# Kernel optimization log

Measured on AMD Instinct MI355X. Metric: run time of the kernel, lower is better.

The kernel has to match this reference:

```python
import jax, jax.numpy as jnp
import numpy as np

DIM = 2048
N_HEADS = 32
N_KV_HEADS = 8
HEAD_DIM = DIM // N_HEADS  # 64
ROPE_BASE = 10000
B, S = 2, 2048


def rope_cos_sin(seq_len, head_dim, base=ROPE_BASE):
    # theta: [head_dim//2]
    theta = 1.0 / (base ** (jnp.arange(0, head_dim, 2, dtype=jnp.float32) / head_dim))
    idx_theta = jnp.arange(seq_len, dtype=jnp.float32)[:, None] * theta[None, :]  # [s, hd/2]
    return jnp.cos(idx_theta), jnp.sin(idx_theta)


def apply_rope(t, cos, sin):
    # t: [b, s, h, hd]; cos/sin: [s, hd/2]
    b, s, h, hd = t.shape
    t2 = t.reshape(b, s, h, hd // 2, 2)
    x0, x1 = t2[..., 0], t2[..., 1]
    c = cos[None, :, None, :]
    sn = sin[None, :, None, :]
    out = jnp.stack([x0 * c - x1 * sn, x1 * c + x0 * sn], axis=-1)
    return out.reshape(b, s, h, hd)


def setup_inputs() -> dict:
    key = jax.random.key(0)
    k1, k2, k3 = jax.random.split(key, 3)
    x = jax.random.normal(k1, (B, S, DIM), dtype=jnp.float32)
    # packed projection weight, stored [in, out]; torch Linear would be its transpose
    packed = DIM + 2 * N_KV_HEADS * HEAD_DIM  # 3072
    w_qkv = jax.random.normal(k2, (DIM, packed), dtype=jnp.float32) * (DIM ** -0.5)
    w_out = jax.random.normal(k3, (DIM, DIM), dtype=jnp.float32) * (DIM ** -0.5)
    return {"x": x, "w_qkv": w_qkv, "w_out": w_out}


def reference(x, w_qkv, w_out):
    b, s, e = x.shape
    hd = HEAD_DIM
    kv_size = N_KV_HEADS * hd
    qkv = x @ w_qkv  # [b, s, dim + 2*kv]
    q = qkv[..., :DIM].reshape(b, s, N_HEADS, hd)
    k = qkv[..., DIM:DIM + kv_size].reshape(b, s, N_KV_HEADS, hd)
    v = qkv[..., DIM + kv_size:].reshape(b, s, N_KV_HEADS, hd)

    cos, sin = rope_cos_sin(s, hd)
    q = apply_rope(q, cos, sin)
    k = apply_rope(k, cos, sin)

    # GQA: group query heads per kv head
    g = N_HEADS // N_KV_HEADS
    q = q.transpose(0, 2, 1, 3).reshape(b, N_KV_HEADS, g, s, hd)  # [b, kh, g, s, hd]
    k = k.transpose(0, 2, 1, 3)  # [b, kh, s, hd]
    v = v.transpose(0, 2, 1, 3)

    scale = 1.0 / jnp.sqrt(jnp.float32(hd))
    scores = jnp.einsum('bkgqd,bktd->bkgqt', q, k) * scale  # [b, kh, g, s, s]
    causal = jnp.tril(jnp.ones((s, s), dtype=bool))
    scores = jnp.where(causal[None, None, None], scores, jnp.finfo(scores.dtype).min)
    probs = jax.nn.softmax(scores, axis=-1)
    attn = jnp.einsum('bkgqt,bktd->bkgqd', probs, v)  # [b, kh, g, s, hd]
    attn = attn.reshape(b, N_HEADS, s, hd).transpose(0, 2, 1, 3).reshape(b, s, DIM)
    return attn @ w_out
```

## Files before the change

### kernel.cpp

```cpp
#include <hip/hip_runtime.h>
#include <hip/hip_bf16.h>
#include <cstdint>
#include <cstddef>

#define DIME 2048
#define NH 32
#define NKV 8
#define HD 64
#define BB 2
#define SSEQ 2048
#define PACKED (DIME + 2*NKV*HD)
#define MTOT (BB*SSEQ)

typedef __attribute__((ext_vector_type(8))) short bf16x8;
typedef __attribute__((ext_vector_type(4))) float f32x4;
typedef __attribute__((ext_vector_type(16))) float f32x16;
typedef __attribute__((ext_vector_type(4))) unsigned u32x4;

__device__ __forceinline__ short f2b(float f) {
  unsigned u = __builtin_bit_cast(unsigned, f);
  u += 0x7fffu + ((u >> 16) & 1u);
  return (short)(u >> 16);
}
__device__ __forceinline__ float b2f(short s) {
  unsigned u = ((unsigned)(unsigned short)s) << 16;
  return __builtin_bit_cast(float, u);
}
__device__ __forceinline__ unsigned cvt_pk(float lo, float hi) {
  unsigned r;
  asm("v_cvt_pk_bf16_f32 %0, %1, %2" : "=v"(r) : "v"(lo), "v"(hi));
  return r;
}

__device__ __forceinline__ void gload_lds16(const void* g, void* l) {
  __builtin_amdgcn_global_load_lds(
      (const __attribute__((address_space(1))) void*)g,
      (__attribute__((address_space(3))) void*)l, 16, 0, 0);
}

__global__ __launch_bounds__(256) void cast_bf16(const float* __restrict__ in,
                                                 short* __restrict__ out, int n4) {
  int i = blockIdx.x * blockDim.x + threadIdx.x;
  int stride = gridDim.x * blockDim.x;
  for (; i < n4; i += stride) {
    float4 v = ((const float4*)in)[i];
    short4 o;
    o.x = f2b(v.x); o.y = f2b(v.y); o.z = f2b(v.z); o.w = f2b(v.w);
    ((short4*)out)[i] = o;
  }
}

__global__ __launch_bounds__(256) void transpose_cast(const float* __restrict__ in,
                                                      short* __restrict__ out,
                                                      int R, int C) {
  __shared__ float tile[32][33];
  int bx = blockIdx.x * 32;
  int by = blockIdx.y * 32;
  int tx = threadIdx.x;
  int ty = threadIdx.y;
  #pragma unroll
  for (int j = 0; j < 4; ++j)
    tile[ty + j*8][tx] = in[(size_t)(by + ty + j*8) * C + bx + tx];
  __syncthreads();
  #pragma unroll
  for (int j = 0; j < 4; ++j)
    out[(size_t)(bx + ty + j*8) * R + by + tx] = f2b(tile[tx][ty + j*8]);
}

__global__ __launch_bounds__(256) void rope_table(float* __restrict__ ctab,
                                                  float* __restrict__ stab) {
  int t = blockIdx.x * blockDim.x + threadIdx.x;
  int s = t >> 5, i = t & 31;
  float theta = 1.0f / powf(10000.0f, (float)(2 * i) * (1.0f / (float)HD));
  float ang = (float)s * theta;
  float sn, cs;
  sincosf(ang, &sn, &cs);
  ctab[t] = cs;
  stab[t] = sn;
}

template<bool BF16_OUT>
__global__ __launch_bounds__(256) void gemm_bt(const short* __restrict__ A,
                                               const short* __restrict__ BT,
                                               void* __restrict__ Cout,
                                               int M, int N, int K) {
  __shared__ __align__(16) short lds[2][2][2][4096];
  const int tid = threadIdx.x;
  const int l = tid & 63, w = tid >> 6;
  const int lr = l & 15, lg = l >> 4;
  const int wm = w >> 1, wn = w & 1;
  const int bm = blockIdx.x * 128, bn = blockIdx.y * 128;
  const int NT = K >> 6;

  const int srow = w * 16 + (l >> 2);
  const int scol = (l & 3) * 8;

  auto stage = [&](int t, int c) {
    const int k0 = t << 6;
    #pragma unroll
    for (int s = 0; s < 2; ++s)
      #pragma unroll
      for (int j = 0; j < 2; ++j) {
        gload_lds16(A  + (size_t)(bm + j * 64 + srow) * K + k0 + s * 32 + scol,
                    &lds[c][0][s][(j * 256 + w * 64) * 8]);
        gload_lds16(BT + (size_t)(bn + j * 64 + srow) * K + k0 + s * 32 + scol,
                    &lds[c][1][s][(j * 256 + w * 64) * 8]);
      }
  };

  f32x4 acc[4][4];
  #pragma unroll
  for (int m = 0; m < 4; ++m)
    #pragma unroll
    for (int n = 0; n < 4; ++n) {
      f32x4 z = {0.f, 0.f, 0.f, 0.f};
      acc[m][n] = z;
    }

  stage(0, 0);
  stage(1, 1);
  asm volatile("s_waitcnt vmcnt(8)" ::: "memory");
  __builtin_amdgcn_sched_barrier(0);
  __builtin_amdgcn_s_barrier();

  for (int t = 0; t < NT; ++t) {
    const int c = t & 1;
    bf16x8 af[4][2], bfr[4][2];
    #pragma unroll
    for (int m = 0; m < 4; ++m)
      #pragma unroll
      for (int ks = 0; ks < 2; ++ks)
        af[m][ks] = *(const bf16x8*)&lds[c][0][ks][((wm * 64 + m * 16 + lr) * 4 + lg) * 8];
    #pragma unroll
    for (int n = 0; n < 4; ++n)
      #pragma unroll
      for (int ks = 0; ks < 2; ++ks)
        bfr[n][ks] = *(const bf16x8*)&lds[c][1][ks][((wn * 64 + n * 16 + lr) * 4 + lg) * 8];
    asm volatile("s_waitcnt lgkmcnt(0)" ::: "memory");
    __builtin_amdgcn_sched_barrier(0);
    __builtin_amdgcn_s_barrier();
    if (t + 2 < NT) stage(t + 2, c);
    __builtin_amdgcn_s_setprio(1);
    #pragma unroll
    for (int m = 0; m < 4; ++m)
      #pragma unroll
      for (int n = 0; n < 4; ++n) {
        acc[m][n] = __builtin_amdgcn_mfma_f32_16x16x32_bf16(af[m][0], bfr[n][0], acc[m][n], 0, 0, 0);
        acc[m][n] = __builtin_amdgcn_mfma_f32_16x16x32_bf16(af[m][1], bfr[n][1], acc[m][n], 0, 0, 0);
      }
    __builtin_amdgcn_s_setprio(0);
    if (t + 2 < NT) {
      asm volatile("s_waitcnt vmcnt(8)" ::: "memory");
    } else if (t + 1 < NT) {
      asm volatile("s_waitcnt vmcnt(0)" ::: "memory");
    }
    __builtin_amdgcn_sched_barrier(0);
    __builtin_amdgcn_s_barrier();
  }

  #pragma unroll
  for (int m = 0; m < 4; ++m)
    #pragma unroll
    for (int n = 0; n < 4; ++n)
      #pragma unroll
      for (int r = 0; r < 4; ++r) {
        int row = bm + wm * 64 + m * 16 + lg * 4 + r;
        int col = bn + wn * 64 + n * 16 + lr;
        if (BF16_OUT)
          ((short*)Cout)[(size_t)row * N + col] = f2b(acc[m][n][r]);
        else
          ((float*)Cout)[(size_t)row * N + col] = acc[m][n][r];
      }
}

__global__ __launch_bounds__(256) void rope_split(const short* __restrict__ qkv,
                                                  const float* __restrict__ ctab,
                                                  const float* __restrict__ stab,
                                                  short* __restrict__ Qo,
                                                  short* __restrict__ Ko) {
  int w = threadIdx.x >> 6, l = threadIdx.x & 63;
  int job = blockIdx.x * 4 + w;
  int b = job / (SSEQ * 40);
  int rem = job % (SSEQ * 40);
  int s = rem / 40;
  int hh = rem % 40;
  size_t base = (size_t)(b * SSEQ + s) * PACKED;
  int off = (hh < 32) ? (hh * HD + l) : (DIME + (hh - 32) * HD + l);
  float x = b2f(qkv[base + off]);
  float other = __shfl_xor(x, 1);
  int i = l >> 1;
  float cs = ctab[s * 32 + i], sn = stab[s * 32 + i];
  float o = (l & 1) ? (x * cs + other * sn) : (x * cs - other * sn);
  if (hh < 32) {
    o *= 0.180336880f;
    Qo[((size_t)(b * NH + hh) * SSEQ + s) * HD + l] = f2b(o);
  } else {
    Ko[((size_t)(b * NKV + (hh - 32)) * SSEQ + s) * HD + l] = f2b(o);
  }
}

__global__ __launch_bounds__(256) void v_transpose(const short* __restrict__ qkv,
                                                   short* __restrict__ VT) {
  __shared__ __align__(16) short tile[64][72];
  int bkv = blockIdx.x >> 5;
  int st = blockIdx.x & 31;
  int s0 = st * 64;
  int t = threadIdx.x;
  int srow = t >> 2, dq = (t & 3) * 16;
  size_t rowbase = (size_t)((bkv >> 3) * SSEQ + s0 + srow) * PACKED
                   + (DIME + NKV * HD) + (bkv & 7) * HD + dq;
  bf16x8 v0 = *(const bf16x8*)&qkv[rowbase];
  bf16x8 v1 = *(const bf16x8*)&qkv[rowbase + 8];
  #pragma unroll
  for (int j = 0; j < 8; ++j) tile[dq + j][srow] = v0[j];
  #pragma unroll
  for (int j = 0; j < 8; ++j) tile[dq + 8 + j][srow] = v1[j];
  __syncthreads();
  int d = t >> 2, sq = (t & 3) * 16;
  size_t obase = ((size_t)bkv * HD + d) * SSEQ + s0 + sq;
  *(bf16x8*)&VT[obase]     = *(const bf16x8*)&tile[d][sq];
  *(bf16x8*)&VT[obase + 8] = *(const bf16x8*)&tile[d][sq + 8];
}

__global__ __launch_bounds__(512) void attn_fwd(const short* __restrict__ Q,
                                                const short* __restrict__ K,
                                                const short* __restrict__ VT,
                                                short* __restrict__ Aout) {
  __shared__ __align__(16) short Ks[2][4096];
  __shared__ __align__(16) short Vs[2][4096];
  const int tid = threadIdx.x, l = tid & 63, w = tid >> 6;
  const int l31 = l & 31;
  const int hi = l >> 5;
  const int qb = 7 - (int)(blockIdx.x >> 6);
  const int bh = blockIdx.x & 63;
  const int b = bh >> 5, hh = bh & 31, kvh = hh >> 2;
  const short* Qp = Q + (size_t)(b * NH + hh) * SSEQ * HD;
  const short* Kp = K + (size_t)(b * NKV + kvh) * SSEQ * HD;
  const short* Vp = VT + (size_t)(b * NKV + kvh) * HD * SSEQ;
  const int q0 = qb * 256 + w * 32;
  const int qrow = q0 + l31;

  const int srow = tid >> 3;
  const int ssl = (tid & 7) ^ (srow & 7);
  auto stage = [&](int t, int c) {
    const int kv0s = t * 64;
    gload_lds16(Kp + (size_t)(kv0s + srow) * HD + ssl * 8, &Ks[c][w * 512]);
    gload_lds16(Vp + (size_t)srow * SSEQ + kv0s + ssl * 8, &Vs[c][w * 512]);
  };

  bf16x8 qf[4];
  #pragma unroll
  for (int ks = 0; ks < 4; ++ks)
    qf[ks] = *(const bf16x8*)&Qp[(size_t)qrow * HD + ks * 16 + hi * 8];

  f32x16 O0, O1;
  #pragma unroll
  for (int r = 0; r < 16; ++r) { O0[r] = 0.f; O1[r] = 0.f; }
  float lsum = 0.f;

  auto compute = [&](int c, int kv0) {
    bf16x8 kf0[4], kf1[4];
    #pragma unroll
    for (int ks = 0; ks < 4; ++ks) {
      kf0[ks] = *(const bf16x8*)&Ks[c][(l31 * 8 + (((ks << 1) + hi) ^ (l31 & 7))) * 8];
      kf1[ks] = *(const bf16x8*)&Ks[c][((32 + l31) * 8 + (((ks << 1) + hi) ^ (l31 & 7))) * 8];
    }
    f32x16 sacc[2];
    #pragma unroll
    for (int r = 0; r < 16; ++r) { sacc[0][r] = -20.f; sacc[1][r] = -20.f; }
    #pragma unroll
    for (int ks = 0; ks < 4; ++ks) {
      sacc[0] = __builtin_amdgcn_mfma_f32_32x32x16_bf16(kf0[ks], qf[ks], sacc[0], 0, 0, 0);
      sacc[1] = __builtin_amdgcn_mfma_f32_32x32x16_bf16(kf1[ks], qf[ks], sacc[1], 0, 0, 0);
    }
    bf16x8 vf0[4], vf1[4];
    #pragma unroll
    for (int ks = 0; ks < 4; ++ks) {
      vf0[ks] = *(const bf16x8*)&Vs[c][(l31 * 8 + (((ks << 1) + hi) ^ (l31 & 7))) * 8];
      vf1[ks] = *(const bf16x8*)&Vs[c][((32 + l31) * 8 + (((ks << 1) + hi) ^ (l31 & 7))) * 8];
    }
    if (kv0 + 63 > q0) {
      #pragma unroll
      for (int n = 0; n < 2; ++n)
        #pragma unroll
        for (int r = 0; r < 16; ++r) {
          int kvg = kv0 + n * 32 + ((r & 3) + 8 * (r >> 2)) + 4 * hi;
          if (kvg > qrow) sacc[n][r] = -3.0e38f;
        }
    }
    float ls0 = 0.f, ls1 = 0.f;
    #pragma unroll
    for (int r = 0; r < 16; ++r) {
      float e0 = exp2f(sacc[0][r]);
      float e1 = exp2f(sacc[1][r]);
      sacc[0][r] = e0;
      sacc[1][r] = e1;
      ls0 += e0;
      ls1 += e1;
    }
    lsum += ls0 + ls1;
    bf16x8 pa[4];
    #pragma unroll
    for (int n = 0; n < 2; ++n)
      #pragma unroll
      for (int s = 0; s < 2; ++s) {
        const int r0 = s * 8;
        unsigned A1 = cvt_pk(sacc[n][r0 + 0], sacc[n][r0 + 1]);
        unsigned B1 = cvt_pk(sacc[n][r0 + 4], sacc[n][r0 + 5]);
        unsigned A2 = cvt_pk(sacc[n][r0 + 2], sacc[n][r0 + 3]);
        unsigned B2 = cvt_pk(sacc[n][r0 + 6], sacc[n][r0 + 7]);
        unsigned shB1 = (unsigned)__shfl_xor((int)B1, 32);
        unsigned shA1 = (unsigned)__shfl_xor((int)A1, 32);
        unsigned shB2 = (unsigned)__shfl_xor((int)B2, 32);
        unsigned shA2 = (unsigned)__shfl_xor((int)A2, 32);
        u32x4 words;
        words[0] = hi ? shB1 : A1;
        words[1] = hi ? shB2 : A2;
        words[2] = hi ? B1 : shA1;
        words[3] = hi ? B2 : shA2;
        pa[n * 2 + s] = __builtin_bit_cast(bf16x8, words);
      }
    #pragma unroll
    for (int ks = 0; ks < 4; ++ks) {
      O0 = __builtin_amdgcn_mfma_f32_32x32x16_bf16(pa[ks], vf0[ks], O0, 0, 0, 0);
      O1 = __builtin_amdgcn_mfma_f32_32x32x16_bf16(pa[ks], vf1[ks], O1, 0, 0, 0);
    }
  };

  const int NT = (qb + 1) * 4;
  stage(0, 0);
  for (int t = 0; t < NT; ++t) {
    const int c = t & 1;
    if (t + 1 < NT) {
      stage(t + 1, c ^ 1);
      asm volatile("s_waitcnt vmcnt(2)" ::: "memory");
    } else {
      asm volatile("s_waitcnt vmcnt(0)" ::: "memory");
    }
    __builtin_amdgcn_sched_barrier(0);
    __builtin_amdgcn_s_barrier();
    const int kv0 = t * 64;
    if (kv0 <= q0 + 31) compute(c, kv0);
    __builtin_amdgcn_s_barrier();
  }

  lsum += __shfl_xor(lsum, 32);
  float inv = 1.0f / lsum;
  #pragma unroll
  for (int r = 0; r < 16; ++r) {
    int crow = (r & 3) + 8 * (r >> 2) + 4 * hi;
    float iq = __shfl(inv, crow);
    int qg = q0 + crow;
    size_t base = (size_t)(b * SSEQ + qg) * DIME + hh * HD;
    Aout[base + l31]      = f2b(O0[r] * iq);
    Aout[base + 32 + l31] = f2b(O1[r] * iq);
  }
}

extern "C" void kernel_launch(void* const* d_in, const int* in_sizes, int n_in,
                              void* d_out, int out_size, void* d_ws, size_t ws_size,
                              hipStream_t stream) {
  const float* x     = (const float*)d_in[0];
  const float* w_qkv = (const float*)d_in[1];
  const float* w_out = (const float*)d_in[2];
  float* out = (float*)d_out;

  char* ws = (char*)d_ws;
  size_t off = 0;
  auto alloc = [&](size_t bytes) -> void* {
    void* p = ws + off;
    off += (bytes + 255) & ~(size_t)255;
    return p;
  };
  short* xb    = (short*)alloc((size_t)MTOT * DIME * 2);
  short* wqkvT = (short*)alloc((size_t)PACKED * DIME * 2);
  short* woutT = (short*)alloc((size_t)DIME * DIME * 2);
  short* qkv   = (short*)alloc((size_t)MTOT * PACKED * 2);
  short* Qb    = (short*)alloc((size_t)BB * NH * SSEQ * HD * 2);
  short* Kb    = (short*)alloc((size_t)BB * NKV * SSEQ * HD * 2);
  short* VTb   = (short*)alloc((size_t)BB * NKV * HD * SSEQ * 2);
  float* ctab  = (float*)alloc((size_t)SSEQ * 32 * 4);
  float* stab  = (float*)alloc((size_t)SSEQ * 32 * 4);
  short* attnb = qkv;

  cast_bf16<<<2048, 256, 0, stream>>>(x, xb, MTOT * DIME / 4);
  transpose_cast<<<dim3(PACKED / 32, DIME / 32), dim3(32, 8), 0, stream>>>(w_qkv, wqkvT, DIME, PACKED);
  transpose_cast<<<dim3(DIME / 32, DIME / 32), dim3(32, 8), 0, stream>>>(w_out, woutT, DIME, DIME);
  rope_table<<<(SSEQ * 32) / 256, 256, 0, stream>>>(ctab, stab);

  gemm_bt<true><<<dim3(MTOT / 128, PACKED / 128), 256, 0, stream>>>(xb, wqkvT, qkv, MTOT, PACKED, DIME);

  rope_split<<<(BB * SSEQ * 40) / 4, 256, 0, stream>>>(qkv, ctab, stab, Qb, Kb);
  v_transpose<<<BB * NKV * (SSEQ / 64), 256, 0, stream>>>(qkv, VTb);

  attn_fwd<<<512, 512, 0, stream>>>(Qb, Kb, VTb, attnb);

  gemm_bt<false><<<dim3(MTOT / 128, DIME / 128), 256, 0, stream>>>(attnb, woutT, out, MTOT, DIME, DIME);
}
```

Before: 222.2 us.

## Fuse RoPE, head split and V transpose into QKV GEMM epilogue

The QKV projection GEMM now applies RoPE and the query scale in its epilogue and writes Q, K and transposed V directly in head-major layouts. This removes the separate rope_split and v_transpose kernels and the round trip of the packed qkv buffer through global memory. The attention grid also reorders query blocks, interleaving heavy and light causal tiles to balance the load. In exchange, the epilogue does scattered stores, shuffles and table loads, and needs a separate attention output buffer.

```diff
diff --git a/kernel.cpp b/kernel.cpp
--- a/kernel.cpp
+++ b/kernel.cpp
@@ -79,11 +79,10 @@
   stab[t] = sn;
 }
 
-template<bool BF16_OUT>
-__global__ __launch_bounds__(256) void gemm_bt(const short* __restrict__ A,
-                                               const short* __restrict__ BT,
-                                               void* __restrict__ Cout,
-                                               int M, int N, int K) {
+__global__ __launch_bounds__(256) void gemm_bt_f32(const short* __restrict__ A,
+                                                   const short* __restrict__ BT,
+                                                   float* __restrict__ Cout,
+                                                   int M, int N, int K) {
   __shared__ __align__(16) short lds[2][2][2][4096];
   const int tid = threadIdx.x;
   const int l = tid & 63, w = tid >> 6;
@@ -166,60 +165,151 @@
       for (int r = 0; r < 4; ++r) {
         int row = bm + wm * 64 + m * 16 + lg * 4 + r;
         int col = bn + wn * 64 + n * 16 + lr;
-        if (BF16_OUT)
-          ((short*)Cout)[(size_t)row * N + col] = f2b(acc[m][n][r]);
-        else
-          ((float*)Cout)[(size_t)row * N + col] = acc[m][n][r];
-      }
-}
-
-__global__ __launch_bounds__(256) void rope_split(const short* __restrict__ qkv,
-                                                  const float* __restrict__ ctab,
-                                                  const float* __restrict__ stab,
-                                                  short* __restrict__ Qo,
-                                                  short* __restrict__ Ko) {
-  int w = threadIdx.x >> 6, l = threadIdx.x & 63;
-  int job = blockIdx.x * 4 + w;
-  int b = job / (SSEQ * 40);
-  int rem = job % (SSEQ * 40);
-  int s = rem / 40;
-  int hh = rem % 40;
-  size_t base = (size_t)(b * SSEQ + s) * PACKED;
-  int off = (hh < 32) ? (hh * HD + l) : (DIME + (hh - 32) * HD + l);
-  float x = b2f(qkv[base + off]);
-  float other = __shfl_xor(x, 1);
-  int i = l >> 1;
-  float cs = ctab[s * 32 + i], sn = stab[s * 32 + i];
-  float o = (l & 1) ? (x * cs + other * sn) : (x * cs - other * sn);
-  if (hh < 32) {
-    o *= 0.180336880f;
-    Qo[((size_t)(b * NH + hh) * SSEQ + s) * HD + l] = f2b(o);
+        Cout[(size_t)row * N + col] = acc[m][n][r];
+      }
+}
+
+__global__ __launch_bounds__(256) void gemm_qkv_fused(const short* __restrict__ A,
+                                                      const short* __restrict__ BT,
+                                                      const float* __restrict__ ctab,
+                                                      const float* __restrict__ stab,
+                                                      short* __restrict__ Qo,
+                                                      short* __restrict__ Ko,
+                                                      short* __restrict__ VT) {
+  __shared__ __align__(16) short lds[2][2][2][4096];
+  const int tid = threadIdx.x;
+  const int l = tid & 63, w = tid >> 6;
+  const int lr = l & 15, lg = l >> 4;
+  const int wm = w >> 1, wn = w & 1;
+  const int bm = blockIdx.x * 128, bn = blockIdx.y * 128;
+  const int K = DIME;
+  const int NT = K >> 6;
+
+  const int srow = w * 16 + (l >> 2);
+  const int scol = (l & 3) * 8;
+
+  auto stage = [&](int t, int c) {
+    const int k0 = t << 6;
+    #pragma unroll
+    for (int s = 0; s < 2; ++s)
+      #pragma unroll
+      for (int j = 0; j < 2; ++j) {
+        gload_lds16(A  + (size_t)(bm + j * 64 + srow) * K + k0 + s * 32 + scol,
+                    &lds[c][0][s][(j * 256 + w * 64) * 8]);
+        gload_lds16(BT + (size_t)(bn + j * 64 + srow) * K + k0 + s * 32 + scol,
+                    &lds[c][1][s][(j * 256 + w * 64) * 8]);
+      }
+  };
+
+  f32x4 acc[4][4];
+  #pragma unroll
+  for (int m = 0; m < 4; ++m)
+    #pragma unroll
+    for (int n = 0; n < 4; ++n) {
+      f32x4 z = {0.f, 0.f, 0.f, 0.f};
+      acc[m][n] = z;
+    }
+
+  stage(0, 0);
+  stage(1, 1);
+  asm volatile("s_waitcnt vmcnt(8)" ::: "memory");
+  __builtin_amdgcn_sched_barrier(0);
+  __builtin_amdgcn_s_barrier();
+
+  for (int t = 0; t < NT; ++t) {
+    const int c = t & 1;
+    bf16x8 af[4][2], bfr[4][2];
+    #pragma unroll
+    for (int m = 0; m < 4; ++m)
+      #pragma unroll
+      for (int ks = 0; ks < 2; ++ks)
+        af[m][ks] = *(const bf16x8*)&lds[c][0][ks][((wm * 64 + m * 16 + lr) * 4 + lg) * 8];
+    #pragma unroll
+    for (int n = 0; n < 4; ++n)
+      #pragma unroll
+      for (int ks = 0; ks < 2; ++ks)
+        bfr[n][ks] = *(const bf16x8*)&lds[c][1][ks][((wn * 64 + n * 16 + lr) * 4 + lg) * 8];
+    asm volatile("s_waitcnt lgkmcnt(0)" ::: "memory");
+    __builtin_amdgcn_sched_barrier(0);
+    __builtin_amdgcn_s_barrier();
+    if (t + 2 < NT) stage(t + 2, c);
+    __builtin_amdgcn_s_setprio(1);
+    #pragma unroll
+    for (int m = 0; m < 4; ++m)
+      #pragma unroll
+      for (int n = 0; n < 4; ++n) {
+        acc[m][n] = __builtin_amdgcn_mfma_f32_16x16x32_bf16(af[m][0], bfr[n][0], acc[m][n], 0, 0, 0);
+        acc[m][n] = __builtin_amdgcn_mfma_f32_16x16x32_bf16(af[m][1], bfr[n][1], acc[m][n], 0, 0, 0);
+      }
+    __builtin_amdgcn_s_setprio(0);
+    if (t + 2 < NT) {
+      asm volatile("s_waitcnt vmcnt(8)" ::: "memory");
+    } else if (t + 1 < NT) {
+      asm volatile("s_waitcnt vmcnt(0)" ::: "memory");
+    }
+    __builtin_amdgcn_sched_barrier(0);
+    __builtin_amdgcn_s_barrier();
+  }
+
+  const int col0 = bn + wn * 64;
+  const int rowb = bm + wm * 64;
+  if (bn < DIME) {
+    #pragma unroll
+    for (int m = 0; m < 4; ++m)
+      #pragma unroll
+      for (int n = 0; n < 4; ++n) {
+        const int col = col0 + n * 16 + lr;
+        const int h = col >> 6, d = col & 63;
+        const int ti = d >> 1;
+        #pragma unroll
+        for (int r = 0; r < 4; ++r) {
+          const int row = rowb + m * 16 + lg * 4 + r;
+          const int bb = row >> 11, s = row & 2047;
+          float val = acc[m][n][r];
+          float oth = __shfl_xor(val, 1);
+          float cs = ctab[s * 32 + ti], snv = stab[s * 32 + ti];
+          float o = (d & 1) ? (val * cs + oth * snv) : (val * cs - oth * snv);
+          o *= 0.180336880f;
+          Qo[((size_t)(bb * NH + h) * SSEQ + s) * HD + d] = f2b(o);
+        }
+      }
+  } else if (bn < DIME + 512) {
+    #pragma unroll
+    for (int m = 0; m < 4; ++m)
+      #pragma unroll
+      for (int n = 0; n < 4; ++n) {
+        const int col = col0 + n * 16 + lr;
+        const int kvh = (col - DIME) >> 6, d = col & 63;
+        const int ti = d >> 1;
+        #pragma unroll
+        for (int r = 0; r < 4; ++r) {
+          const int row = rowb + m * 16 + lg * 4 + r;
+          const int bb = row >> 11, s = row & 2047;
+          float val = acc[m][n][r];
+          float oth = __shfl_xor(val, 1);
+          float cs = ctab[s * 32 + ti], snv = stab[s * 32 + ti];
+          float o = (d & 1) ? (val * cs + oth * snv) : (val * cs - oth * snv);
+          Ko[((size_t)(bb * NKV + kvh) * SSEQ + s) * HD + d] = f2b(o);
+        }
+      }
   } else {
-    Ko[((size_t)(b * NKV + (hh - 32)) * SSEQ + s) * HD + l] = f2b(o);
-  }
-}
-
-__global__ __launch_bounds__(256) void v_transpose(const short* __restrict__ qkv,
-                                                   short* __restrict__ VT) {
-  __shared__ __align__(16) short tile[64][72];
-  int bkv = blockIdx.x >> 5;
-  int st = blockIdx.x & 31;
-  int s0 = st * 64;
-  int t = threadIdx.x;
-  int srow = t >> 2, dq = (t & 3) * 16;
-  size_t rowbase = (size_t)((bkv >> 3) * SSEQ + s0 + srow) * PACKED
-                   + (DIME + NKV * HD) + (bkv & 7) * HD + dq;
-  bf16x8 v0 = *(const bf16x8*)&qkv[rowbase];
-  bf16x8 v1 = *(const bf16x8*)&qkv[rowbase + 8];
-  #pragma unroll
-  for (int j = 0; j < 8; ++j) tile[dq + j][srow] = v0[j];
-  #pragma unroll
-  for (int j = 0; j < 8; ++j) tile[dq + 8 + j][srow] = v1[j];
-  __syncthreads();
-  int d = t >> 2, sq = (t & 3) * 16;
-  size_t obase = ((size_t)bkv * HD + d) * SSEQ + s0 + sq;
-  *(bf16x8*)&VT[obase]     = *(const bf16x8*)&tile[d][sq];
-  *(bf16x8*)&VT[obase + 8] = *(const bf16x8*)&tile[d][sq + 8];
+    #pragma unroll
+    for (int m = 0; m < 4; ++m) {
+      const int row0 = rowb + m * 16 + lg * 4;
+      const int bb = row0 >> 11, s = row0 & 2047;
+      #pragma unroll
+      for (int n = 0; n < 4; ++n) {
+        const int cc = col0 - (DIME + 512) + n * 16 + lr;
+        const int kvh = cc >> 6, d = cc & 63;
+        short4 o4;
+        o4.x = f2b(acc[m][n][0]);
+        o4.y = f2b(acc[m][n][1]);
+        o4.z = f2b(acc[m][n][2]);
+        o4.w = f2b(acc[m][n][3]);
+        *(short4*)&VT[((size_t)(bb * NKV + kvh) * HD + d) * SSEQ + s] = o4;
+      }
+    }
+  }
 }
 
 __global__ __launch_bounds__(512) void attn_fwd(const short* __restrict__ Q,
@@ -231,7 +321,8 @@
   const int tid = threadIdx.x, l = tid & 63, w = tid >> 6;
   const int l31 = l & 31;
   const int hi = l >> 5;
-  const int qb = 7 - (int)(blockIdx.x >> 6);
+  const int j = (int)(blockIdx.x >> 6);
+  const int qb = (j < 4) ? (7 - j) : (j - 4);
   const int bh = blockIdx.x & 63;
   const int b = bh >> 5, hh = bh & 31, kvh = hh >> 2;
   const short* Qp = Q + (size_t)(b * NH + hh) * SSEQ * HD;
@@ -375,25 +466,22 @@
   short* xb    = (short*)alloc((size_t)MTOT * DIME * 2);
   short* wqkvT = (short*)alloc((size_t)PACKED * DIME * 2);
   short* woutT = (short*)alloc((size_t)DIME * DIME * 2);
-  short* qkv   = (short*)alloc((size_t)MTOT * PACKED * 2);
   short* Qb    = (short*)alloc((size_t)BB * NH * SSEQ * HD * 2);
   short* Kb    = (short*)alloc((size_t)BB * NKV * SSEQ * HD * 2);
   short* VTb   = (short*)alloc((size_t)BB * NKV * HD * SSEQ * 2);
+  short* attnb = (short*)alloc((size_t)MTOT * DIME * 2);
   float* ctab  = (float*)alloc((size_t)SSEQ * 32 * 4);
   float* stab  = (float*)alloc((size_t)SSEQ * 32 * 4);
-  short* attnb = qkv;
 
   cast_bf16<<<2048, 256, 0, stream>>>(x, xb, MTOT * DIME / 4);
   transpose_cast<<<dim3(PACKED / 32, DIME / 32), dim3(32, 8), 0, stream>>>(w_qkv, wqkvT, DIME, PACKED);
   transpose_cast<<<dim3(DIME / 32, DIME / 32), dim3(32, 8), 0, stream>>>(w_out, woutT, DIME, DIME);
   rope_table<<<(SSEQ * 32) / 256, 256, 0, stream>>>(ctab, stab);
 
-  gemm_bt<true><<<dim3(MTOT / 128, PACKED / 128), 256, 0, stream>>>(xb, wqkvT, qkv, MTOT, PACKED, DIME);
-
-  rope_split<<<(BB * SSEQ * 40) / 4, 256, 0, stream>>>(qkv, ctab, stab, Qb, Kb);
-  v_transpose<<<BB * NKV * (SSEQ / 64), 256, 0, stream>>>(qkv, VTb);
+  gemm_qkv_fused<<<dim3(MTOT / 128, PACKED / 128), 256, 0, stream>>>(
+      xb, wqkvT, ctab, stab, Qb, Kb, VTb);
 
   attn_fwd<<<512, 512, 0, stream>>>(Qb, Kb, VTb, attnb);
 
-  gemm_bt<false><<<dim3(MTOT / 128, DIME / 128), 256, 0, stream>>>(attnb, woutT, out, MTOT, DIME, DIME);
-}
+  gemm_bt_f32<<<dim3(MTOT / 128, DIME / 128), 256, 0, stream>>>(attnb, woutT, out, MTOT, DIME, DIME);
+}
```

Result: no change. 219.8 us (-1.1%).
